# Optimization experiments

Measured on AMD Instinct MI355X. Metric: run time of the kernel, lower is better.

Reference implementation:

```python
import jax, jax.numpy as jnp
import numpy as np

N_NODES = 50000


def gcn_conv(x, src, dst, norm, W, b, n):
    # PyG GCNConv: out = A_hat @ (x W) + b, with A_hat = D^-1/2 (A+I) D^-1/2
    h = x @ W                                   # [N, out]
    msgs = norm[:, None] * h[src]               # [E+N, out]
    out = jax.ops.segment_sum(msgs, dst, num_segments=n)
    return out + b


def _norm_and_loops(edge_index, n):
    # add self loops
    loops = jnp.arange(n, dtype=edge_index.dtype)
    src = jnp.concatenate([edge_index[0], loops])
    dst = jnp.concatenate([edge_index[1], loops])
    ones = jnp.ones(src.shape[0], dtype=jnp.float32)
    deg = jax.ops.segment_sum(ones, dst, num_segments=n)
    dinv = jnp.where(deg > 0, jax.lax.rsqrt(jnp.maximum(deg, 1e-12)), 0.0)
    norm = dinv[src] * dinv[dst]
    return src, dst, norm


def setup_inputs() -> dict:
    key = jax.random.key(0)
    k1, k2, k3, k4, k5, k6 = jax.random.split(key, 6)
    F_in, H, C = 1433, 128, 7
    x = jax.random.normal(k1, (N_NODES, F_in), dtype=jnp.float32)
    edge_index = jax.random.randint(k2, (2, 1600000), 0, N_NODES, dtype=jnp.int64)
    W1 = jax.random.normal(k3, (F_in, H), dtype=jnp.float32) / np.sqrt(F_in)
    b1 = jnp.zeros((H,), dtype=jnp.float32)
    W2 = jax.random.normal(k4, (H, C), dtype=jnp.float32) / np.sqrt(H)
    b2 = jnp.zeros((C,), dtype=jnp.float32)
    return {"x": x, "edge_index": edge_index, "W1": W1, "b1": b1, "W2": W2, "b2": b2}


def reference(x, edge_index, W1, b1, W2, b2):
    n = x.shape[0]
    src, dst, norm = _norm_and_loops(edge_index, n)
    h = gcn_conv(x, src, dst, norm, W1, b1, n)
    h = jax.nn.relu(h)
    # dropout p=0.5 is identity in eval mode
    out = gcn_conv(h, src, dst, norm, W2, b2, n)
    return out
```

## Files before the change

kernel.cpp:

```cpp
#include <hip/hip_runtime.h>
#include <hip/hip_bf16.h>

typedef __attribute__((ext_vector_type(8))) short short8_t;
typedef __attribute__((ext_vector_type(4))) float f32x4;
typedef float f32x4u __attribute__((ext_vector_type(4), aligned(4)));

#define NNODES 50000
#define FIN 1433
#define HID 128
#define NCLS 7
#define KT1 23
#define BK 64
#define BM 128
#define CAP 96

static __device__ __forceinline__ unsigned short f2bf(float f) {
    union { float f; unsigned int u; } v; v.f = f;
    unsigned int u = v.u;
    u += 0x7FFFu + ((u >> 16) & 1u);
    return (unsigned short)(u >> 16);
}
static __device__ __forceinline__ float u2f(unsigned int u) {
    union { unsigned int u; float f; } v; v.u = u; return v.f;
}

__global__ void prep_w1(const float* __restrict__ W1, unsigned short* __restrict__ W1s) {
    int tid = blockIdx.x * 512 + threadIdx.x;
    if (tid >= KT1 * 1024) return;
    int kt = tid >> 10, seg = tid & 1023;
    int c = seg & 127, g = seg >> 7;
    int kb = kt * BK + g * 8;
    unsigned int w[4];
    #pragma unroll
    for (int p = 0; p < 4; ++p) {
        int k0 = kb + p * 2, k1 = kb + p * 2 + 1;
        unsigned short lo = (k0 < FIN) ? f2bf(W1[(size_t)k0 * HID + c]) : (unsigned short)0;
        unsigned short hi = (k1 < FIN) ? f2bf(W1[(size_t)k1 * HID + c]) : (unsigned short)0;
        w[p] = (unsigned int)lo | ((unsigned int)hi << 16);
    }
    uint4* dstp = (uint4*)(W1s + (size_t)tid * 8);
    uint4 val; val.x = w[0]; val.y = w[1]; val.z = w[2]; val.w = w[3];
    *dstp = val;
}

__global__ __launch_bounds__(512, 4) void gemm_fill(const float* __restrict__ x,
                                                    const unsigned short* __restrict__ W1s,
                                                    unsigned short* __restrict__ h, int M,
                                                    const int* __restrict__ src,
                                                    const int* __restrict__ dst, int E,
                                                    int* __restrict__ cnt,
                                                    int* __restrict__ csr_f,
                                                    int* __restrict__ ovf_cnt,
                                                    int2* __restrict__ ovf, int gb) {
    __shared__ unsigned short As[2][8192];
    __shared__ unsigned short Bs[3][8192];

    if (blockIdx.x >= gb) {
        int bid = blockIdx.x - gb;
        int i = (bid * 512 + (int)threadIdx.x) * 8;
        int lim = min(i + 8, E);
        for (int e = i; e < lim; ++e) {
            int d = dst[e], s = src[e];
            int pos = atomicAdd(&cnt[d], 1);
            if (pos < CAP) csr_f[d * CAP + pos] = s;
            else { int op = atomicAdd(ovf_cnt, 1); ovf[op] = make_int2(d, s); }
        }
        return;
    }

    const int t = threadIdx.x;
    const int wave = t >> 6, lane = t & 63;
    const int wm = wave >> 1, wn = wave & 1;
    const int r = lane & 15, u = lane >> 4;
    const int rowBase = blockIdx.x * BM;
    f32x4 acc[2][4] = {};

    float4 areg[4];

    auto issueA = [&](int kt) {
        int k0 = kt * BK;
        #pragma unroll
        for (int i = 0; i < 4; ++i) {
            int quad = i * 512 + t;
            int row = quad >> 4, kq = quad & 15;
            int gr = rowBase + row;
            int gk = k0 + kq * 4;
            if (gr < M && gk + 3 < FIN) {
                f32x4u v = __builtin_nontemporal_load((const f32x4u*)(x + (size_t)gr * FIN + gk));
                areg[i].x = v.x; areg[i].y = v.y; areg[i].z = v.z; areg[i].w = v.w;
            } else {
                areg[i].x = (gr < M && gk + 0 < FIN) ? x[(size_t)gr * FIN + gk + 0] : 0.f;
                areg[i].y = (gr < M && gk + 1 < FIN) ? x[(size_t)gr * FIN + gk + 1] : 0.f;
                areg[i].z = (gr < M && gk + 2 < FIN) ? x[(size_t)gr * FIN + gk + 2] : 0.f;
                areg[i].w = (gr < M && gk + 3 < FIN) ? x[(size_t)gr * FIN + gk + 3] : 0.f;
            }
        }
    };
    auto issueB = [&](int kt, int buf) {
        #pragma unroll
        for (int i = 0; i < 2; ++i) {
            const unsigned short* gp = W1s + ((size_t)kt * 1024 + (size_t)(i * 512 + t)) * 8;
            unsigned short* lp = &Bs[buf][(i * 512 + wave * 64) * 8];
            __builtin_amdgcn_global_load_lds(
                (const __attribute__((address_space(1))) unsigned int*)gp,
                (__attribute__((address_space(3))) unsigned int*)lp, 16, 0, 0);
        }
    };
    auto writeA = [&](int buf) {
        #pragma unroll
        for (int i = 0; i < 4; ++i) {
            int quad = i * 512 + t;
            int row = quad >> 4, kq = quad & 15;
            __hip_bfloat162 lo2 = __float22bfloat162_rn(make_float2(areg[i].x, areg[i].y));
            __hip_bfloat162 hi2 = __float22bfloat162_rn(make_float2(areg[i].z, areg[i].w));
            unsigned int ulo, uhi;
            __builtin_memcpy(&ulo, &lo2, 4);
            __builtin_memcpy(&uhi, &hi2, 4);
            unsigned long long pk = ((unsigned long long)uhi << 32) | (unsigned long long)ulo;
            int us = row * 64 + ((kq * 4) ^ ((row & 7) << 3));
            *(unsigned long long*)(&As[buf][us]) = pk;
        }
    };
    auto compute = [&](int abuf, int bbuf) {
        short8_t af[2][2], bfr[2][4];
        #pragma unroll
        for (int ks = 0; ks < 2; ++ks) {
            int g = ks * 4 + u;
            #pragma unroll
            for (int mi = 0; mi < 2; ++mi) {
                int row = wm * 32 + mi * 16 + r;
                int us = row * 64 + ((g * 8) ^ ((row & 7) << 3));
                af[ks][mi] = *(const short8_t*)(&As[abuf][us]);
            }
            #pragma unroll
            for (int ni = 0; ni < 4; ++ni) {
                int c = wn * 64 + ni * 16 + r;
                bfr[ks][ni] = *(const short8_t*)(&Bs[bbuf][g * 1024 + c * 8]);
            }
        }
        #pragma unroll
        for (int ks = 0; ks < 2; ++ks)
            #pragma unroll
            for (int mi = 0; mi < 2; ++mi)
                #pragma unroll
                for (int ni = 0; ni < 4; ++ni)
                    acc[mi][ni] = __builtin_amdgcn_mfma_f32_16x16x32_bf16(af[ks][mi], bfr[ks][ni], acc[mi][ni], 0, 0, 0);
    };

    issueA(0); issueB(0, 0);
    writeA(0);
    issueA(1); issueB(1, 1);
    asm volatile("s_waitcnt vmcnt(6) lgkmcnt(0)" ::: "memory");
    __builtin_amdgcn_sched_barrier(0);
    __builtin_amdgcn_s_barrier();
    __builtin_amdgcn_sched_barrier(0);

    for (int kt = 0; kt < KT1 - 2; ++kt) {
        compute(kt & 1, kt % 3);
        writeA((kt + 1) & 1);
        issueA(kt + 2);
        issueB(kt + 2, (kt + 2) % 3);
        asm volatile("s_waitcnt vmcnt(6) lgkmcnt(0)" ::: "memory");
        __builtin_amdgcn_sched_barrier(0);
        __builtin_amdgcn_s_barrier();
        __builtin_amdgcn_sched_barrier(0);
    }
    {
        const int kt = KT1 - 2;
        compute(kt & 1, kt % 3);
        writeA((kt + 1) & 1);
        __syncthreads();
    }
    compute((KT1 - 1) & 1, (KT1 - 1) % 3);

    #pragma unroll
    for (int mi = 0; mi < 2; ++mi) {
        #pragma unroll
        for (int reg = 0; reg < 4; ++reg) {
            int grow = rowBase + wm * 32 + mi * 16 + u * 4 + reg;
            if (grow < M) {
                #pragma unroll
                for (int ni = 0; ni < 4; ++ni) {
                    int gcol = wn * 64 + ni * 16 + r;
                    h[(size_t)grow * HID + gcol] = f2bf(acc[mi][ni][reg]);
                }
            }
        }
    }
}

__global__ void self_dinv(int* __restrict__ cnt, int* __restrict__ csr_f,
                          float* __restrict__ dinv,
                          int* __restrict__ ovf_cnt, int2* __restrict__ ovf, int n) {
    int i = blockIdx.x * 256 + threadIdx.x;
    if (i >= n) return;
    int c = cnt[i];
    if (c < CAP) csr_f[i * CAP + c] = i;
    else { int op = atomicAdd(ovf_cnt, 1); ovf[op] = make_int2(i, i); }
    cnt[i] = c + 1;
    dinv[i] = rsqrtf((float)(c + 1));
}

__global__ __launch_bounds__(256) void agg1(const unsigned short* __restrict__ h,
                                            const int* __restrict__ cnt,
                                            const int* __restrict__ csr_f,
                                            const float* __restrict__ dinv,
                                            const float* __restrict__ b1,
                                            const float* __restrict__ W2,
                                            const int* __restrict__ ovf_cnt,
                                            const int2* __restrict__ ovf,
                                            float* __restrict__ h2s, int n) {
    __shared__ float W2s[HID * NCLS];
    for (int i = threadIdx.x; i < HID * NCLS; i += 256) W2s[i] = W2[i];
    __syncthreads();
    int wave = threadIdx.x >> 6, lane = threadIdx.x & 63;
    int v = blockIdx.x * 4 + wave;
    if (v >= n) return;
    const int fr = lane & 15, g = lane >> 4;
    int total = cnt[v];
    int inrow = min(total, CAP);
    const int base = v * CAP;
    float acc[8] = {};
    #pragma unroll 4
    for (int j = g; j < inrow; j += 4) {
        int s = csr_f[base + j];
        float ds = dinv[s];
        uint4 q = *(const uint4*)(h + (size_t)s * HID + fr * 8);
        unsigned int w[4] = {q.x, q.y, q.z, q.w};
        #pragma unroll
        for (int p = 0; p < 4; ++p) {
            acc[p * 2 + 0] += ds * u2f(w[p] << 16);
            acc[p * 2 + 1] += ds * u2f(w[p] & 0xffff0000u);
        }
    }
    if (__builtin_expect(total > CAP, 0) && g == 0) {
        int on = *ovf_cnt;
        for (int k = 0; k < on; ++k) {
            int2 pr = ovf[k];
            if (pr.x == v) {
                int s = pr.y;
                float ds = dinv[s];
                uint4 q = *(const uint4*)(h + (size_t)s * HID + fr * 8);
                unsigned int w[4] = {q.x, q.y, q.z, q.w};
                #pragma unroll
                for (int p = 0; p < 4; ++p) {
                    acc[p * 2 + 0] += ds * u2f(w[p] << 16);
                    acc[p * 2 + 1] += ds * u2f(w[p] & 0xffff0000u);
                }
            }
        }
    }
    #pragma unroll
    for (int e = 0; e < 8; ++e) {
        acc[e] += __shfl_xor(acc[e], 16, 64);
        acc[e] += __shfl_xor(acc[e], 32, 64);
    }
    float dv = dinv[v];
    float p[NCLS];
    #pragma unroll
    for (int c = 0; c < NCLS; ++c) p[c] = 0.f;
    #pragma unroll
    for (int e = 0; e < 8; ++e) {
        int f = fr * 8 + e;
        float val = fmaxf(dv * acc[e] + b1[f], 0.f);
        #pragma unroll
        for (int c = 0; c < NCLS; ++c) p[c] += val * W2s[f * NCLS + c];
    }
    #pragma unroll
    for (int off = 8; off >= 1; off >>= 1)
        #pragma unroll
        for (int c = 0; c < NCLS; ++c)
            p[c] += __shfl_xor(p[c], off, 64);
    if (lane == 0) {
        #pragma unroll
        for (int c = 0; c < NCLS; ++c) h2s[(size_t)v * 8 + c] = dv * p[c];
        h2s[(size_t)v * 8 + 7] = 0.f;
    }
}

__global__ __launch_bounds__(256) void agg2(const float* __restrict__ h2s,
                                            const int* __restrict__ cnt,
                                            const int* __restrict__ csr_f,
                                            const float* __restrict__ dinv,
                                            const float* __restrict__ b2,
                                            const int* __restrict__ ovf_cnt,
                                            const int2* __restrict__ ovf,
                                            float* __restrict__ out, int n) {
    int wave = threadIdx.x >> 6, lane = threadIdx.x & 63;
    int half = lane >> 5;
    int c = lane & 7, g = (lane >> 3) & 3;
    int v = blockIdx.x * 8 + wave * 2 + half;
    if (v >= n) return;
    int total = cnt[v];
    int inrow = min(total, CAP);
    const int base = v * CAP;
    float acc = 0.f;
    #pragma unroll 4
    for (int j = g; j < inrow; j += 4) {
        int s = csr_f[base + j];
        acc += h2s[(size_t)s * 8 + c];
    }
    if (__builtin_expect(total > CAP, 0) && g == 0) {
        int on = *ovf_cnt;
        for (int k = 0; k < on; ++k) {
            int2 pr = ovf[k];
            if (pr.x == v) acc += h2s[(size_t)pr.y * 8 + c];
        }
    }
    acc += __shfl_xor(acc, 8, 64);
    acc += __shfl_xor(acc, 16, 64);
    if (g == 0 && c < NCLS) out[(size_t)v * NCLS + c] = dinv[v] * acc + b2[c];
}

extern "C" void kernel_launch(void* const* d_in, const int* in_sizes, int n_in,
                              void* d_out, int out_size, void* d_ws, size_t ws_size,
                              hipStream_t stream) {
    const float* x  = (const float*)d_in[0];
    const int*   ei = (const int*)d_in[1];
    const float* W1 = (const float*)d_in[2];
    const float* b1 = (const float*)d_in[3];
    const float* W2 = (const float*)d_in[4];
    const float* b2 = (const float*)d_in[5];
    float* out = (float*)d_out;

    const int N = NNODES;
    const int E = in_sizes[1] / 2;
    const int* src = ei;
    const int* dst = ei + E;
    const int GB = (N + BM - 1) / BM;
    const int FB = (E + 4095) / 4096;

    char* ws = (char*)d_ws;
    size_t off = 0;
    auto alloc = [&](size_t bytes) {
        void* p = ws + off;
        off += (bytes + 255) & ~(size_t)255;
        return p;
    };
    int*   cnt     = (int*)alloc((size_t)N * 4);
    int*   ovf_cnt = (int*)alloc(4);
    float* dinv    = (float*)alloc((size_t)N * 4);
    int*   csr_f   = (int*)alloc((size_t)N * CAP * 4);
    int2*  ovf     = (int2*)alloc((size_t)4096 * 8);
    unsigned short* W1s = (unsigned short*)alloc((size_t)KT1 * 1024 * 8 * 2);
    unsigned short* h   = (unsigned short*)alloc((size_t)N * HID * 2);
    float* h2s     = (float*)alloc((size_t)N * 8 * 4);

    hipMemsetAsync(cnt, 0, ((char*)ovf_cnt - (char*)cnt) + 256, stream);
    prep_w1<<<(KT1 * 1024 + 511) / 512, 512, 0, stream>>>(W1, W1s);
    gemm_fill<<<GB + FB, 512, 0, stream>>>(x, W1s, h, N, src, dst, E,
                                           cnt, csr_f, ovf_cnt, ovf, GB);
    self_dinv<<<(N + 255) / 256, 256, 0, stream>>>(cnt, csr_f, dinv, ovf_cnt, ovf, N);
    agg1<<<(N + 3) / 4, 256, 0, stream>>>(h, cnt, csr_f, dinv, b1, W2, ovf_cnt, ovf, h2s, N);
    agg2<<<(N + 7) / 8, 256, 0, stream>>>(h2s, cnt, csr_f, dinv, b2, ovf_cnt, ovf, out, N);
}
```

Baseline: 247.4 us.

## Halve GEMM K-tile to 32, shrink LDS, raise occupancy, new A-tile swizzle

Cuts the K tile of the bf16 MFMA GEMM from 64 to 32, so each iteration issues half as many loads and MFMAs and the LDS footprint roughly halves. Launch bounds go from 4 to 8 blocks per CU to take advantage of that. The A tile gets a group-strided XOR swizzle with padding, and the x loads drop the nontemporal hint and per-row bounds checks by clamping the row index. The partial K tail moves into a separate guarded load step. The cost is twice as many barrier-synchronised iterations and tighter register pressure from the higher occupancy target.

```diff
diff --git a/kernel.cpp b/kernel.cpp
--- a/kernel.cpp
+++ b/kernel.cpp
@@ -9,10 +9,11 @@
 #define FIN 1433
 #define HID 128
 #define NCLS 7
-#define KT1 23
-#define BK 64
+#define KT1 45
+#define BK 32
 #define BM 128
 #define CAP 96
+#define GSTR 1040
 
 static __device__ __forceinline__ unsigned short f2bf(float f) {
     union { float f; unsigned int u; } v; v.f = f;
@@ -26,8 +27,8 @@
 
 __global__ void prep_w1(const float* __restrict__ W1, unsigned short* __restrict__ W1s) {
     int tid = blockIdx.x * 512 + threadIdx.x;
-    if (tid >= KT1 * 1024) return;
-    int kt = tid >> 10, seg = tid & 1023;
+    if (tid >= KT1 * 512) return;
+    int kt = tid >> 9, seg = tid & 511;
     int c = seg & 127, g = seg >> 7;
     int kb = kt * BK + g * 8;
     unsigned int w[4];
@@ -43,7 +44,7 @@
     *dstp = val;
 }
 
-__global__ __launch_bounds__(512, 4) void gemm_fill(const float* __restrict__ x,
+__global__ __launch_bounds__(512, 8) void gemm_fill(const float* __restrict__ x,
                                                     const unsigned short* __restrict__ W1s,
                                                     unsigned short* __restrict__ h, int M,
                                                     const int* __restrict__ src,
@@ -52,8 +53,8 @@
                                                     int* __restrict__ csr_f,
                                                     int* __restrict__ ovf_cnt,
                                                     int2* __restrict__ ovf, int gb) {
-    __shared__ unsigned short As[2][8192];
-    __shared__ unsigned short Bs[3][8192];
+    __shared__ unsigned short As[2][4160];
+    __shared__ unsigned short Bs[3][4096];
 
     if (blockIdx.x >= gb) {
         int bid = blockIdx.x - gb;
@@ -75,103 +76,107 @@
     const int rowBase = blockIdx.x * BM;
     f32x4 acc[2][4] = {};
 
-    float4 areg[4];
+    float4 areg[2];
 
     auto issueA = [&](int kt) {
         int k0 = kt * BK;
         #pragma unroll
-        for (int i = 0; i < 4; ++i) {
+        for (int i = 0; i < 2; ++i) {
             int quad = i * 512 + t;
-            int row = quad >> 4, kq = quad & 15;
-            int gr = rowBase + row;
+            int row = quad >> 3, kq = quad & 7;
+            int gr = min(rowBase + row, M - 1);
             int gk = k0 + kq * 4;
-            if (gr < M && gk + 3 < FIN) {
-                f32x4u v = __builtin_nontemporal_load((const f32x4u*)(x + (size_t)gr * FIN + gk));
-                areg[i].x = v.x; areg[i].y = v.y; areg[i].z = v.z; areg[i].w = v.w;
-            } else {
-                areg[i].x = (gr < M && gk + 0 < FIN) ? x[(size_t)gr * FIN + gk + 0] : 0.f;
-                areg[i].y = (gr < M && gk + 1 < FIN) ? x[(size_t)gr * FIN + gk + 1] : 0.f;
-                areg[i].z = (gr < M && gk + 2 < FIN) ? x[(size_t)gr * FIN + gk + 2] : 0.f;
-                areg[i].w = (gr < M && gk + 3 < FIN) ? x[(size_t)gr * FIN + gk + 3] : 0.f;
-            }
+            f32x4u v = *(const f32x4u*)(x + (size_t)gr * FIN + gk);
+            areg[i].x = v.x; areg[i].y = v.y; areg[i].z = v.z; areg[i].w = v.w;
+        }
+    };
+    auto issueA_tail = [&]() {
+        #pragma unroll
+        for (int i = 0; i < 2; ++i) {
+            int quad = i * 512 + t;
+            int row = quad >> 3, kq = quad & 7;
+            int gr = min(rowBase + row, M - 1);
+            int gk = 1408 + kq * 4;
+            const float* p = x + (size_t)gr * FIN;
+            areg[i].x = (gk + 0 < FIN) ? p[gk + 0] : 0.f;
+            areg[i].y = (gk + 1 < FIN) ? p[gk + 1] : 0.f;
+            areg[i].z = (gk + 2 < FIN) ? p[gk + 2] : 0.f;
+            areg[i].w = (gk + 3 < FIN) ? p[gk + 3] : 0.f;
         }
     };
     auto issueB = [&](int kt, int buf) {
+        const unsigned short* gp = W1s + ((size_t)kt * 512 + t) * 8;
+        unsigned short* lp = &Bs[buf][(wave * 64) * 8];
+        __builtin_amdgcn_global_load_lds(
+            (const __attribute__((address_space(1))) unsigned int*)gp,
+            (__attribute__((address_space(3))) unsigned int*)lp, 16, 0, 0);
+    };
+    auto writeA = [&](int buf) {
         #pragma unroll
         for (int i = 0; i < 2; ++i) {
-            const unsigned short* gp = W1s + ((size_t)kt * 1024 + (size_t)(i * 512 + t)) * 8;
-            unsigned short* lp = &Bs[buf][(i * 512 + wave * 64) * 8];
-            __builtin_amdgcn_global_load_lds(
-                (const __attribute__((address_space(1))) unsigned int*)gp,
-                (__attribute__((address_space(3))) unsigned int*)lp, 16, 0, 0);
-        }
-    };
-    auto writeA = [&](int buf) {
-        #pragma unroll
-        for (int i = 0; i < 4; ++i) {
             int quad = i * 512 + t;
-            int row = quad >> 4, kq = quad & 15;
+            int row = quad >> 3, kq = quad & 7;
             __hip_bfloat162 lo2 = __float22bfloat162_rn(make_float2(areg[i].x, areg[i].y));
             __hip_bfloat162 hi2 = __float22bfloat162_rn(make_float2(areg[i].z, areg[i].w));
             unsigned int ulo, uhi;
             __builtin_memcpy(&ulo, &lo2, 4);
             __builtin_memcpy(&uhi, &hi2, 4);
             unsigned long long pk = ((unsigned long long)uhi << 32) | (unsigned long long)ulo;
-            int us = row * 64 + ((kq * 4) ^ ((row & 7) << 3));
+            int g = kq >> 1, half = kq & 1;
+            int us = ((g ^ (row & 3)) * GSTR) + row * 8 + half * 4;
             *(unsigned long long*)(&As[buf][us]) = pk;
         }
     };
-    auto compute = [&](int abuf, int bbuf) {
-        short8_t af[2][2], bfr[2][4];
-        #pragma unroll
-        for (int ks = 0; ks < 2; ++ks) {
-            int g = ks * 4 + u;
+    auto compute = [&](int kt) {
+        const int abuf = kt & 1, bbuf = kt % 3;
+        short8_t af[2], bfr[4];
+        #pragma unroll
+        for (int mi = 0; mi < 2; ++mi) {
+            int row = wm * 32 + mi * 16 + r;
+            int us = ((u ^ (row & 3)) * GSTR) + row * 8;
+            af[mi] = *(const short8_t*)(&As[abuf][us]);
+        }
+        #pragma unroll
+        for (int ni = 0; ni < 4; ++ni) {
+            int c = wn * 64 + ni * 16 + r;
+            bfr[ni] = *(const short8_t*)(&Bs[bbuf][u * 1024 + c * 8]);
+        }
+        #pragma unroll
+        for (int mi = 0; mi < 2; ++mi)
             #pragma unroll
-            for (int mi = 0; mi < 2; ++mi) {
-                int row = wm * 32 + mi * 16 + r;
-                int us = row * 64 + ((g * 8) ^ ((row & 7) << 3));
-                af[ks][mi] = *(const short8_t*)(&As[abuf][us]);
-            }
-            #pragma unroll
-            for (int ni = 0; ni < 4; ++ni) {
-                int c = wn * 64 + ni * 16 + r;
-                bfr[ks][ni] = *(const short8_t*)(&Bs[bbuf][g * 1024 + c * 8]);
-            }
-        }
-        #pragma unroll
-        for (int ks = 0; ks < 2; ++ks)
-            #pragma unroll
-            for (int mi = 0; mi < 2; ++mi)
-                #pragma unroll
-                for (int ni = 0; ni < 4; ++ni)
-                    acc[mi][ni] = __builtin_amdgcn_mfma_f32_16x16x32_bf16(af[ks][mi], bfr[ks][ni], acc[mi][ni], 0, 0, 0);
+            for (int ni = 0; ni < 4; ++ni)
+                acc[mi][ni] = __builtin_amdgcn_mfma_f32_16x16x32_bf16(af[mi], bfr[ni], acc[mi][ni], 0, 0, 0);
     };
 
     issueA(0); issueB(0, 0);
     writeA(0);
     issueA(1); issueB(1, 1);
-    asm volatile("s_waitcnt vmcnt(6) lgkmcnt(0)" ::: "memory");
+    asm volatile("s_waitcnt vmcnt(3) lgkmcnt(0)" ::: "memory");
     __builtin_amdgcn_sched_barrier(0);
     __builtin_amdgcn_s_barrier();
     __builtin_amdgcn_sched_barrier(0);
 
-    for (int kt = 0; kt < KT1 - 2; ++kt) {
-        compute(kt & 1, kt % 3);
+    for (int kt = 0; kt < KT1 - 3; ++kt) {
+        compute(kt);
         writeA((kt + 1) & 1);
         issueA(kt + 2);
         issueB(kt + 2, (kt + 2) % 3);
-        asm volatile("s_waitcnt vmcnt(6) lgkmcnt(0)" ::: "memory");
+        asm volatile("s_waitcnt vmcnt(3) lgkmcnt(0)" ::: "memory");
         __builtin_amdgcn_sched_barrier(0);
         __builtin_amdgcn_s_barrier();
         __builtin_amdgcn_sched_barrier(0);
     }
     {
-        const int kt = KT1 - 2;
-        compute(kt & 1, kt % 3);
-        writeA((kt + 1) & 1);
+        compute(KT1 - 3);
+        writeA((KT1 - 2) & 1);
         __syncthreads();
     }
-    compute((KT1 - 1) & 1, (KT1 - 1) % 3);
+    issueA_tail();
+    issueB(KT1 - 1, (KT1 - 1) % 3);
+    writeA((KT1 - 1) & 1);
+    __syncthreads();
+    compute(KT1 - 2);
+    compute(KT1 - 1);
 
     #pragma unroll
     for (int mi = 0; mi < 2; ++mi) {
@@ -342,12 +347,12 @@
     float* dinv    = (float*)alloc((size_t)N * 4);
     int*   csr_f   = (int*)alloc((size_t)N * CAP * 4);
     int2*  ovf     = (int2*)alloc((size_t)4096 * 8);
-    unsigned short* W1s = (unsigned short*)alloc((size_t)KT1 * 1024 * 8 * 2);
+    unsigned short* W1s = (unsigned short*)alloc((size_t)KT1 * 512 * 8 * 2);
     unsigned short* h   = (unsigned short*)alloc((size_t)N * HID * 2);
     float* h2s     = (float*)alloc((size_t)N * 8 * 4);
 
     hipMemsetAsync(cnt, 0, ((char*)ovf_cnt - (char*)cnt) + 256, stream);
-    prep_w1<<<(KT1 * 1024 + 511) / 512, 512, 0, stream>>>(W1, W1s);
+    prep_w1<<<(KT1 * 512 + 511) / 512, 512, 0, stream>>>(W1, W1s);
     gemm_fill<<<GB + FB, 512, 0, stream>>>(x, W1s, h, N, src, dst, E,
                                            cnt, csr_f, ovf_cnt, ovf, GB);
     self_dinv<<<(N + 255) / 256, 256, 0, stream>>>(cnt, csr_f, dinv, ovf_cnt, ovf, N);
```

Result: faster. 241.0 us (-2.6%).
